# Kernel tuning notes

Hardware: AMD Instinct MI355X
Metric: run time of the kernel (lower is better)

The kernel has to match this reference:

```python
import jax, jax.numpy as jnp
import numpy as np

N_KNN = 16
BN_EPS = 1e-5


def conv1d(x, w, b):
    # x: [B, Cin, N], w: [Cout, Cin], b: [Cout] (1x1 Conv1d)
    return jnp.einsum('oc,bcn->bon', w, x) + b[None, :, None]


def conv2d(x, w, b):
    # x: [B, Cin, N, K], w: [Cout, Cin], b: [Cout] (1x1 Conv2d)
    return jnp.einsum('oc,bcnk->bonk', w, x) + b[None, :, None, None]


def bn2d(x, gamma, beta, mean, var):
    # eval-mode BatchNorm2d over channel axis 1
    scale = (gamma / jnp.sqrt(var + BN_EPS))[None, :, None, None]
    return (x - mean[None, :, None, None]) * scale + beta[None, :, None, None]


def knn_idx(pos, k):
    # pos: [B, 3, N] -> idx: [B, N, K] of k nearest neighbors (incl. self)
    p = jnp.swapaxes(pos, 1, 2)  # [B, N, 3]
    sq = jnp.sum(p * p, axis=-1)  # [B, N]
    d2 = sq[:, :, None] - 2.0 * jnp.einsum('bnd,bmd->bnm', p, p) + sq[:, None, :]
    _, idx = jax.lax.top_k(-d2, k)
    return idx


def group(x, idx):
    # x: [B, C, N], idx: [B, N, K] -> [B, C, N, K] (grouping_operation)
    return jax.vmap(lambda xb, ib: xb[:, ib])(x, idx)


def setup_inputs() -> dict:
    key = jax.random.key(0)
    B, C_OBJ, C_Q, N, DIM, PH, AM = 4, 512, 512, 4096, 128, 64, 4
    ks = jax.random.split(key, 32)
    r = lambda i, sh, s=0.05: jax.random.normal(ks[i], sh, jnp.float32) * s
    inp = {
        'obj_feature': jax.random.normal(ks[0], (B, C_OBJ, N), jnp.float32),
        'pos': jax.random.normal(ks[1], (B, 3, N), jnp.float32),
        'query_points': jax.random.normal(ks[2], (B, C_Q, N), jnp.float32),
        # linear_start_query / linear_start_obj
        'w_sq': r(3, (DIM, C_Q)), 'b_sq': r(4, (DIM,)),
        'w_so': r(5, (DIM, C_OBJ)), 'b_so': r(6, (DIM,)),
        # key / query / value 1x1 convs
        'w_k': r(7, (DIM, DIM)), 'b_k': r(8, (DIM,)),
        'w_q': r(9, (DIM, DIM)), 'b_q': r(10, (DIM,)),
        'w_v': r(11, (DIM, DIM)), 'b_v': r(12, (DIM,)),
        # pos_mlp: Conv2d(3->PH), BN, ReLU, Conv2d(PH->DIM)
        'w_p1': r(13, (PH, 3)), 'b_p1': r(14, (PH,)),
        'g_bn1': 1.0 + r(15, (PH,)), 'be_bn1': r(16, (PH,)),
        'm_bn1': r(17, (PH,)), 'v_bn1': 1.0 + 0.1 * jax.random.uniform(ks[18], (PH,), jnp.float32),
        'w_p2': r(19, (DIM, PH)), 'b_p2': r(20, (DIM,)),
        # attn_mlp: Conv2d(DIM->DIM*AM), BN, ReLU, Conv2d(DIM*AM->DIM)
        'w_a1': r(21, (DIM * AM, DIM)), 'b_a1': r(22, (DIM * AM,)),
        'g_bn2': 1.0 + r(23, (DIM * AM,)), 'be_bn2': r(24, (DIM * AM,)),
        'm_bn2': r(25, (DIM * AM,)), 'v_bn2': 1.0 + 0.1 * jax.random.uniform(ks[26], (DIM * AM,), jnp.float32),
        # linear_end
        'w_e': r(27, (C_OBJ, DIM)), 'b_e': r(28, (C_OBJ,)),
    }
    return inp


def reference(obj_feature, pos, query_points, w_sq, b_sq, w_so, b_so, w_k, b_k,
              w_q, b_q, w_v, b_v, w_p1, b_p1, g_bn1, be_bn1, m_bn1, v_bn1,
              w_p2, b_p2, w_a1, b_a1, g_bn2, be_bn2, m_bn2, v_bn2, w_e, b_e):
    qf = conv1d(query_points, w_sq, b_sq)          # [B, dim, N]
    f = conv1d(obj_feature, w_so, b_so)            # [B, dim, N]
    idx = knn_idx(jax.lax.stop_gradient(pos), N_KNN)  # [B, N, K]
    key_g = group(conv1d(f, w_k, b_k), idx)        # [B, dim, N, K]
    value = conv1d(f, w_v, b_v)                    # [B, dim, N]
    query = conv1d(qf, w_q, b_q)                   # [B, dim, N]
    qk_rel = query[:, :, :, None] - key_g          # [B, dim, N, K]
    pos_rel = pos[:, :, :, None] - group(pos, idx)  # [B, 3, N, K]
    pe = conv2d(jax.nn.relu(bn2d(conv2d(pos_rel, w_p1, b_p1), g_bn1, be_bn1, m_bn1, v_bn1)), w_p2, b_p2)
    attn = conv2d(jax.nn.relu(bn2d(conv2d(qk_rel + pe, w_a1, b_a1), g_bn2, be_bn2, m_bn2, v_bn2)), w_a2_placeholder := w_p2 * 0 + 0, b_p2 * 0) if False else None
    hidden = jax.nn.relu(bn2d(conv2d(qk_rel + pe, w_a1, b_a1), g_bn2, be_bn2, m_bn2, v_bn2))
    attn = jax.nn.softmax(conv2d(hidden, w_a2, b_a2), axis=-1)  # softmax over K
    v = value[:, :, :, None] + pe                  # [B, dim, N, K]
    agg = jnp.sum(attn * v, axis=-1)               # 'b c i j, b c i j -> b c i'
    return conv1d(agg, w_e, b_e)                   # [B, C_obj, N]

# fix: w_a2/b_a2 are parameters; re-declare reference cleanly to include them

def _setup_extra(inp):
    kk = jax.random.split(jax.random.key(7), 2)
    inp['w_a2'] = jax.random.normal(kk[0], (128, 512), jnp.float32) * 0.05
    inp['b_a2'] = jax.random.normal(kk[1], (128,), jnp.float32) * 0.05
    return inp

_orig_setup = setup_inputs

def setup_inputs():
    return _setup_extra(_orig_setup())


def reference(obj_feature, pos, query_points, w_sq, b_sq, w_so, b_so, w_k, b_k,
              w_q, b_q, w_v, b_v, w_p1, b_p1, g_bn1, be_bn1, m_bn1, v_bn1,
              w_p2, b_p2, w_a1, b_a1, g_bn2, be_bn2, m_bn2, v_bn2, w_a2, b_a2,
              w_e, b_e):
    qf = conv1d(query_points, w_sq, b_sq)
    f = conv1d(obj_feature, w_so, b_so)
    idx = knn_idx(jax.lax.stop_gradient(pos), N_KNN)
    key_g = group(conv1d(f, w_k, b_k), idx)
    value = conv1d(f, w_v, b_v)
    query = conv1d(qf, w_q, b_q)
    qk_rel = query[:, :, :, None] - key_g
    pos_rel = pos[:, :, :, None] - group(pos, idx)
    pe = conv2d(jax.nn.relu(bn2d(conv2d(pos_rel, w_p1, b_p1), g_bn1, be_bn1, m_bn1, v_bn1)), w_p2, b_p2)
    hidden = jax.nn.relu(bn2d(conv2d(qk_rel + pe, w_a1, b_a1), g_bn2, be_bn2, m_bn2, v_bn2))
    attn = jax.nn.softmax(conv2d(hidden, w_a2, b_a2), axis=-1)
    v = value[:, :, :, None] + pe
    agg = jnp.sum(attn * v, axis=-1)
    return conv1d(agg, w_e, b_e)
```

## Files before the change

kernel.cpp:

```cpp
#include <hip/hip_runtime.h>

typedef __bf16 bf16;
typedef __bf16 bf16x8 __attribute__((ext_vector_type(8)));
typedef __bf16 bf16x4 __attribute__((ext_vector_type(4)));
typedef __bf16 bf16x2 __attribute__((ext_vector_type(2)));
typedef float f32x4 __attribute__((ext_vector_type(4)));

#define MFMA16(a,b,c) __builtin_amdgcn_mfma_f32_16x16x32_bf16((a),(b),(c),0,0,0)

#define NPTS 4096
#define CIN 512
#define DIM 128
#define PH 64
#define HID 512

#define OFF_WQS 0u
#define OFF_WKO (128u*1024u)
#define OFF_WVO (256u*1024u)
#define OFF_BQS (384u*1024u)
#define OFF_BKO (385u*1024u)
#define OFF_BVO (386u*1024u)
#define OFF_S1  (387u*1024u)
#define OFF_T1  (388u*1024u)
#define OFF_S2  (389u*1024u)
#define OFF_T2  (391u*1024u)
#define OFF_CW  (400u*1024u)
#define OFF_QT  (1u<<20)
#define OFF_KT  (OFF_QT + (4u<<20))
#define OFF_VT  (OFF_QT + (8u<<20))
#define OFF_IDX (OFF_QT + (12u<<20))
#define WS_NEED (OFF_QT + (13u<<20))

struct P {
  const float* in[31];
  char* ws;
  float* out;
};

__global__ __launch_bounds__(256) void k_fold(P p) {
  int tid = blockIdx.x*256 + threadIdx.x;
  char* ws = p.ws;
  if (tid < 196608) {
    int m_id = tid >> 16, o = (tid >> 9) & 127, c = tid & 511;
    const float* A  = m_id==0 ? p.in[9] : (m_id==1 ? p.in[7] : p.in[11]);
    const float* Bm = (m_id==0) ? p.in[3] : p.in[5];
    float acc = 0.f;
    #pragma unroll 8
    for (int m=0;m<128;m++) acc += A[o*128+m] * Bm[m*512+c];
    bf16* outw = (bf16*)(ws + (m_id==0?OFF_WQS: m_id==1?OFF_WKO:OFF_WVO));
    outw[o*512+c] = (bf16)acc;
  } else if (tid < 196992) {
    int t = tid - 196608; int m_id = t >> 7, o = t & 127;
    const float* A  = m_id==0 ? p.in[9] : (m_id==1 ? p.in[7] : p.in[11]);
    const float* bb = (m_id==0) ? p.in[4] : p.in[6];
    const float* bs = m_id==0 ? p.in[10] : (m_id==1 ? p.in[8] : p.in[12]);
    float acc = bs[o];
    for (int m=0;m<128;m++) acc += A[o*128+m] * bb[m];
    float* ob = (float*)(ws + (m_id==0?OFF_BQS: m_id==1?OFF_BKO:OFF_BVO));
    ob[o] = acc;
  } else if (tid < 197056) {
    int i = tid - 196992;
    float s = p.in[15][i] * rsqrtf(p.in[18][i] + 1e-5f);
    ((float*)(ws+OFF_S1))[i] = s;
    ((float*)(ws+OFF_T1))[i] = (p.in[14][i] - p.in[17][i])*s + p.in[16][i];
  } else if (tid < 197568) {
    int i = tid - 197056;
    float s = p.in[23][i] * rsqrtf(p.in[26][i] + 1e-5f);
    ((float*)(ws+OFF_S2))[i] = s;
    ((float*)(ws+OFF_T2))[i] = (p.in[22][i] - p.in[25][i])*s + p.in[24][i];
  } else if (tid < 223168) {
    int e0 = (tid - 197568) * 8;
    const float* src; int base;
    if (e0 < 8192)        { src = p.in[19]; base = 0; }
    else if (e0 < 73728)  { src = p.in[21]; base = 8192; }
    else if (e0 < 139264) { src = p.in[29]; base = 73728; }
    else                  { src = p.in[27]; base = 139264; }
    const float* sp = src + (e0 - base);
    f32x4 a = *(const f32x4*)sp, b2 = *(const f32x4*)(sp+4);
    bf16x8 o8;
    o8[0]=(bf16)a[0]; o8[1]=(bf16)a[1]; o8[2]=(bf16)a[2]; o8[3]=(bf16)a[3];
    o8[4]=(bf16)b2[0]; o8[5]=(bf16)b2[1]; o8[6]=(bf16)b2[2]; o8[7]=(bf16)b2[3];
    *(bf16x8*)((bf16*)(ws+OFF_CW) + e0) = o8;
  }
}

__global__ __launch_bounds__(256) void k_knn(P p) {
  int lane = threadIdx.x & 63, w = threadIdx.x >> 6;
  int ig = blockIdx.x*4 + w;
  int b = ig >> 12, n = ig & 4095;
  const float* pb = p.in[1] + b*3*NPTS;
  float qx = pb[n], qy = pb[NPTS+n], qz = pb[2*NPTS+n];
  float sqn = __fadd_rn(__fadd_rn(__fmul_rn(qx,qx), __fmul_rn(qy,qy)), __fmul_rn(qz,qz));
  float d2a[64];
  #pragma unroll
  for (int t=0;t<64;t++) {
    int j = t*64 + lane;
    float xj=pb[j], yj=pb[NPTS+j], zj=pb[2*NPTS+j];
    float sqj = __fadd_rn(__fadd_rn(__fmul_rn(xj,xj), __fmul_rn(yj,yj)), __fmul_rn(zj,zj));
    float dot = __fadd_rn(__fadd_rn(__fmul_rn(qx,xj), __fmul_rn(qy,yj)), __fmul_rn(qz,zj));
    d2a[t] = __fadd_rn(__fsub_rn(sqn, __fmul_rn(2.f,dot)), sqj);
  }
  int* op = (int*)(p.ws + OFF_IDX) + ig*16;
  long long prev = -1ll;
  for (int r=0;r<16;r++) {
    long long best = 0x7fffffffffffffffll;
    #pragma unroll
    for (int t=0;t<64;t++) {
      long long key = ((long long)(int)__float_as_uint(d2a[t]) << 32) | (long long)(t*64+lane);
      if (key > prev && key < best) best = key;
    }
    #pragma unroll
    for (int off=32; off>0; off>>=1) {
      long long o = __shfl_xor(best, off);
      best = best < o ? best : o;
    }
    prev = best;
    if (lane==0) op[r] = (int)best & 4095;
  }
}

__global__ __launch_bounds__(256) void k_qkv(P p) {
  int mat = blockIdx.z, b = blockIdx.y, n0 = blockIdx.x*64;
  int tid = threadIdx.x, lane = tid&63, w = tid>>6;
  const float* in = (mat==0 ? p.in[2] : p.in[0]) + b*CIN*NPTS;
  const bf16* W = (const bf16*)(p.ws + (mat==0?OFF_WQS: mat==1?OFF_WKO:OFF_WVO));
  const float* bias = (const float*)(p.ws + (mat==0?OFF_BQS: mat==1?OFF_BKO:OFF_BVO));
  bf16* outT = (bf16*)(p.ws + (mat==0?OFF_QT: mat==1?OFF_KT:OFF_VT)) + (b*NPTS + n0)*DIM;
  __shared__ __align__(16) bf16 Bl[64*40];
  f32x4 acc[8] = {};
  for (int ks=0; ks<16; ks++) {
    int c0 = ks*32;
    {
      int cc = tid>>3, nn0 = (tid&7)*8;
      const float* sp = in + (c0+cc)*NPTS + n0 + nn0;
      f32x4 a = *(const f32x4*)sp, b2 = *(const f32x4*)(sp+4);
      Bl[(nn0+0)*40+cc]=(bf16)a[0];  Bl[(nn0+1)*40+cc]=(bf16)a[1];
      Bl[(nn0+2)*40+cc]=(bf16)a[2];  Bl[(nn0+3)*40+cc]=(bf16)a[3];
      Bl[(nn0+4)*40+cc]=(bf16)b2[0]; Bl[(nn0+5)*40+cc]=(bf16)b2[1];
      Bl[(nn0+6)*40+cc]=(bf16)b2[2]; Bl[(nn0+7)*40+cc]=(bf16)b2[3];
    }
    __syncthreads();
    int ncol = w*16 + (lane&15);
    bf16x8 bfr = *(const bf16x8*)(&Bl[ncol*40 + (lane>>4)*8]);
    #pragma unroll
    for (int ot=0;ot<8;ot++) {
      bf16x8 af = *(const bf16x8*)(W + (ot*16 + (lane&15))*CIN + c0 + (lane>>4)*8);
      acc[ot] = MFMA16(af, bfr, acc[ot]);
    }
    __syncthreads();
  }
  int o0 = (lane>>4)*4;
  int nloc = w*16 + (lane&15);
  #pragma unroll
  for (int ot=0;ot<8;ot++) {
    f32x4 bs = *(const f32x4*)(bias + ot*16 + o0);
    bf16x4 st;
    st[0]=(bf16)(acc[ot][0]+bs[0]); st[1]=(bf16)(acc[ot][1]+bs[1]);
    st[2]=(bf16)(acc[ot][2]+bs[2]); st[3]=(bf16)(acc[ot][3]+bs[3]);
    *(bf16x4*)(outT + nloc*DIM + ot*16 + o0) = st;
  }
}

__global__ __launch_bounds__(512) void k_fused(P p) {
  int b = blockIdx.y, pt0 = blockIdx.x*8;
  int tid=threadIdx.x, lane=tid&63, w=tid>>6;
  char* ws = p.ws;
  const bf16* qT = (const bf16*)(ws+OFF_QT) + b*NPTS*DIM;
  const bf16* kT = (const bf16*)(ws+OFF_KT) + b*NPTS*DIM;
  const bf16* vT = (const bf16*)(ws+OFF_VT) + b*NPTS*DIM;
  const int* idxg = (const int*)(ws+OFF_IDX) + (b*NPTS + pt0)*16;
  const bf16* wp2b = (const bf16*)(ws+OFF_CW);
  const bf16* wa1b = wp2b + 8192;
  const bf16* wa2b = wa1b + 65536;
  const bf16* web  = wa2b + 65536;
  __shared__ __align__(16) bf16 Xl[128*136];
  __shared__ __align__(16) bf16 HT[128*72];
  __shared__ __align__(16) bf16 aggl[16*136];
  __shared__ float prl[128][4];
  __shared__ int idxl[128];

  if (tid < 128) {
    int pt = tid>>4;
    int j = idxg[tid] & 4095;
    idxl[tid] = j;
    const float* pb = p.in[1] + b*3*NPTS;
    int n = pt0+pt;
    prl[tid][0] = pb[n]        - pb[j];
    prl[tid][1] = pb[NPTS+n]   - pb[NPTS+j];
    prl[tid][2] = pb[2*NPTS+n] - pb[2*NPTS+j];
  } else if (tid >= 256 && tid < 392) {
    f32x4 z = {};
    *(f32x4*)((char*)aggl + 2176 + (tid-256)*16) = z;
  }
  __syncthreads();

  {
    int col = tid & 127, mb = (tid>>7)*16;
    float r0=prl[col][0], r1=prl[col][1], r2=prl[col][2];
    const float* wp1 = p.in[13];
    const float* s1 = (const float*)(ws+OFF_S1);
    const float* t1 = (const float*)(ws+OFF_T1);
    #pragma unroll
    for (int i=0;i<16;i+=2) {
      int m = mb+i;
      float x0 = wp1[m*3]*r0   + wp1[m*3+1]*r1 + wp1[m*3+2]*r2;
      float x1 = wp1[m*3+3]*r0 + wp1[m*3+4]*r1 + wp1[m*3+5]*r2;
      bf16x2 pk;
      pk[0] = (bf16)fmaxf(0.f, x0*s1[m]   + t1[m]);
      pk[1] = (bf16)fmaxf(0.f, x1*s1[m+1] + t1[m+1]);
      *(bf16x2*)(&HT[col*72 + m]) = pk;
    }
  }
  __syncthreads();

  {
    f32x4 acc[8] = {};
    int crow = w*16 + (lane&15);
    #pragma unroll
    for (int ksx=0; ksx<2; ksx++) {
      int m0 = ksx*32 + (lane>>4)*8;
      bf16x8 af = *(const bf16x8*)(wp2b + crow*PH + m0);
      #pragma unroll
      for (int nt=0; nt<8; nt++) {
        int col = nt*16 + (lane&15);
        bf16x8 bfr = *(const bf16x8*)(&HT[col*72 + m0]);
        acc[nt] = MFMA16(af, bfr, acc[nt]);
      }
    }
    int c0 = w*16 + (lane>>4)*4;
    f32x4 bp4 = *(const f32x4*)(p.in[20] + c0);
    #pragma unroll
    for (int nt=0; nt<8; nt++) {
      int col = nt*16 + (lane&15);
      int j = idxl[col];
      int n = pt0 + nt;
      bf16x4 q4 = *(const bf16x4*)(qT + n*DIM + c0);
      bf16x4 k4 = *(const bf16x4*)(kT + j*DIM + c0);
      bf16x4 st;
      #pragma unroll
      for (int r=0;r<4;r++)
        st[r] = (bf16)((float)q4[r] - (float)k4[r] + acc[nt][r] + bp4[r]);
      *(bf16x4*)(&Xl[col*136 + c0]) = st;
    }
  }
  __syncthreads();

  f32x4 S[8] = {};
  const float* s2 = (const float*)(ws+OFF_S2);
  const float* t2 = (const float*)(ws+OFF_T2);
  for (int ch=0; ch<8; ch++) {
    f32x4 acc1[4] = {};
    int mtw = w & 3, nbase = (w>>2)*4;
    int hrow = ch*64 + mtw*16 + (lane&15);
    #pragma unroll
    for (int ksx=0; ksx<4; ksx++) {
      bf16x8 af = *(const bf16x8*)(wa1b + hrow*DIM + ksx*32 + (lane>>4)*8);
      #pragma unroll
      for (int i=0; i<4; i++) {
        int col = (nbase+i)*16 + (lane&15);
        bf16x8 bfr = *(const bf16x8*)(&Xl[col*136 + ksx*32 + (lane>>4)*8]);
        acc1[i] = MFMA16(af, bfr, acc1[i]);
      }
    }
    int h0 = ch*64 + mtw*16 + (lane>>4)*4;
    int h0loc = mtw*16 + (lane>>4)*4;
    f32x4 sv = *(const f32x4*)(s2 + h0);
    f32x4 tv = *(const f32x4*)(t2 + h0);
    #pragma unroll
    for (int i=0;i<4;i++) {
      int col = (nbase+i)*16 + (lane&15);
      bf16x4 st;
      st[0]=(bf16)fmaxf(0.f, acc1[i][0]*sv[0]+tv[0]);
      st[1]=(bf16)fmaxf(0.f, acc1[i][1]*sv[1]+tv[1]);
      st[2]=(bf16)fmaxf(0.f, acc1[i][2]*sv[2]+tv[2]);
      st[3]=(bf16)fmaxf(0.f, acc1[i][3]*sv[3]+tv[3]);
      *(bf16x4*)(&HT[col*72 + h0loc]) = st;
    }
    __syncthreads();
    int orow = w*16 + (lane&15);
    #pragma unroll
    for (int ksx=0; ksx<2; ksx++) {
      bf16x8 af = *(const bf16x8*)(wa2b + orow*HID + ch*64 + ksx*32 + (lane>>4)*8);
      #pragma unroll
      for (int nt=0; nt<8; nt++) {
        int col = nt*16 + (lane&15);
        bf16x8 bfr = *(const bf16x8*)(&HT[col*72 + ksx*32 + (lane>>4)*8]);
        S[nt] = MFMA16(af, bfr, S[nt]);
      }
    }
    __syncthreads();
  }

  {
    int c0 = w*16 + (lane>>4)*4;
    #pragma unroll
    for (int nt=0; nt<8; nt++) {
      f32x4 s = S[nt];
      float at[4];
      #pragma unroll
      for (int r=0;r<4;r++) {
        float mx = s[r];
        #pragma unroll
        for (int mk=8; mk; mk>>=1) mx = fmaxf(mx, __shfl_xor(mx, mk));
        float e = __expf(s[r]-mx);
        float sum = e;
        #pragma unroll
        for (int mk=8; mk; mk>>=1) sum += __shfl_xor(sum, mk);
        at[r] = e / sum;
      }
      int col = nt*16 + (lane&15);
      int j = idxl[col];
      int n = pt0 + nt;
      bf16x4 x4 = *(const bf16x4*)(&Xl[col*136 + c0]);
      bf16x4 q4 = *(const bf16x4*)(qT + n*DIM + c0);
      bf16x4 k4 = *(const bf16x4*)(kT + j*DIM + c0);
      bf16x4 v4 = *(const bf16x4*)(vT + n*DIM + c0);
      float ag[4];
      #pragma unroll
      for (int r=0;r<4;r++) {
        float vpe = (float)v4[r] + (float)x4[r] - (float)q4[r] + (float)k4[r];
        float cab = at[r]*vpe;
        #pragma unroll
        for (int mk=8; mk; mk>>=1) cab += __shfl_xor(cab, mk);
        ag[r] = cab;
      }
      if ((lane&15)==0) {
        bf16x4 st;
        st[0]=(bf16)ag[0]; st[1]=(bf16)ag[1]; st[2]=(bf16)ag[2]; st[3]=(bf16)ag[3];
        *(bf16x4*)(&aggl[nt*136 + c0]) = st;
      }
    }
  }
  __syncthreads();

  {
    const float* be = p.in[28];
    f32x4 acc5[4] = {};
    #pragma unroll
    for (int ksx=0; ksx<4; ksx++) {
      int pcol = lane&15;
      bf16x8 bfr = *(const bf16x8*)(&aggl[pcol*136 + ksx*32 + (lane>>4)*8]);
      #pragma unroll
      for (int i=0;i<4;i++) {
        int e = (w*4+i)*16 + (lane&15);
        bf16x8 af = *(const bf16x8*)(web + e*DIM + ksx*32 + (lane>>4)*8);
        acc5[i] = MFMA16(af, bfr, acc5[i]);
      }
    }
    int ptc = lane&15;
    if (ptc < 8) {
      int n = pt0 + ptc;
      #pragma unroll
      for (int i=0;i<4;i++) {
        int e0 = (w*4+i)*16 + (lane>>4)*4;
        f32x4 be4 = *(const f32x4*)(be + e0);
        #pragma unroll
        for (int r=0;r<4;r++)
          p.out[(b*CIN + e0+r)*NPTS + n] = acc5[i][r] + be4[r];
      }
    }
  }
}

extern "C" void kernel_launch(void* const* d_in, const int* in_sizes, int n_in,
                              void* d_out, int out_size, void* d_ws, size_t ws_size,
                              hipStream_t stream) {
  if (ws_size < WS_NEED || n_in < 31) return;
  P p;
  for (int i=0;i<31;i++) p.in[i] = (const float*)d_in[i];
  p.ws = (char*)d_ws;
  p.out = (float*)d_out;
  k_fold<<<872, 256, 0, stream>>>(p);
  k_knn<<<4096, 256, 0, stream>>>(p);
  k_qkv<<<dim3(64, 4, 3), 256, 0, stream>>>(p);
  k_fused<<<dim3(512, 4), 512, 0, stream>>>(p);
}
```

Measured before the change: 457.3 us.

## Rework kNN selection and retile attention MLP with 2D warp tiles and DPP reductions

The kNN kernel now stores distances as order-preserving 32-bit unsigned keys. Each round takes a single unsigned min scan and then clears the chosen element, replacing the previous 64-bit key comparisons against the last selected value. In the fused kernel, the attention MLP is retiled so each warp computes a 32x64 block over 128-wide hidden chunks (4 chunks instead of 8). This halves the barrier count and reuses each loaded B fragment across two A rows. Softmax and aggregation reductions use DPP row rotations instead of shuffles, at the cost of a larger HT shared buffer and a switch-based dynamic register clear.

After: 483.3 us. +5.7%, slower.

```diff
diff --git a/kernel.cpp b/kernel.cpp
--- a/kernel.cpp
+++ b/kernel.cpp
@@ -36,6 +36,16 @@
   char* ws;
   float* out;
 };
+
+template<int C> __device__ __forceinline__ float rorf(float x){
+  return __int_as_float(__builtin_amdgcn_mov_dpp(__float_as_int(x), 0x120|C, 0xF, 0xF, true));
+}
+__device__ __forceinline__ float red16max(float x){
+  x=fmaxf(x,rorf<1>(x)); x=fmaxf(x,rorf<2>(x)); x=fmaxf(x,rorf<4>(x)); x=fmaxf(x,rorf<8>(x)); return x;
+}
+__device__ __forceinline__ float red16sum(float x){
+  x+=rorf<1>(x); x+=rorf<2>(x); x+=rorf<4>(x); x+=rorf<8>(x); return x;
+}
 
 __global__ __launch_bounds__(256) void k_fold(P p) {
   int tid = blockIdx.x*256 + threadIdx.x;
@@ -91,31 +101,53 @@
   const float* pb = p.in[1] + b*3*NPTS;
   float qx = pb[n], qy = pb[NPTS+n], qz = pb[2*NPTS+n];
   float sqn = __fadd_rn(__fadd_rn(__fmul_rn(qx,qx), __fmul_rn(qy,qy)), __fmul_rn(qz,qz));
-  float d2a[64];
+  unsigned u[64];
   #pragma unroll
   for (int t=0;t<64;t++) {
     int j = t*64 + lane;
     float xj=pb[j], yj=pb[NPTS+j], zj=pb[2*NPTS+j];
     float sqj = __fadd_rn(__fadd_rn(__fmul_rn(xj,xj), __fmul_rn(yj,yj)), __fmul_rn(zj,zj));
     float dot = __fadd_rn(__fadd_rn(__fmul_rn(qx,xj), __fmul_rn(qy,yj)), __fmul_rn(qz,zj));
-    d2a[t] = __fadd_rn(__fsub_rn(sqn, __fmul_rn(2.f,dot)), sqj);
+    float d2 = __fadd_rn(__fsub_rn(sqn, __fmul_rn(2.f,dot)), sqj);
+    unsigned bbits = __float_as_uint(d2);
+    u[t] = bbits ^ (((unsigned)((int)bbits >> 31)) | 0x80000000u);
   }
   int* op = (int*)(p.ws + OFF_IDX) + ig*16;
-  long long prev = -1ll;
+  int tsel_s = 64; bool mine = false;
+  #pragma unroll 1
   for (int r=0;r<16;r++) {
-    long long best = 0x7fffffffffffffffll;
+    switch (tsel_s) {
+#define CLR(T) case T: u[T] = mine ? 0xFFFFFFFFu : u[T]; break;
+      CLR(0) CLR(1) CLR(2) CLR(3) CLR(4) CLR(5) CLR(6) CLR(7)
+      CLR(8) CLR(9) CLR(10) CLR(11) CLR(12) CLR(13) CLR(14) CLR(15)
+      CLR(16) CLR(17) CLR(18) CLR(19) CLR(20) CLR(21) CLR(22) CLR(23)
+      CLR(24) CLR(25) CLR(26) CLR(27) CLR(28) CLR(29) CLR(30) CLR(31)
+      CLR(32) CLR(33) CLR(34) CLR(35) CLR(36) CLR(37) CLR(38) CLR(39)
+      CLR(40) CLR(41) CLR(42) CLR(43) CLR(44) CLR(45) CLR(46) CLR(47)
+      CLR(48) CLR(49) CLR(50) CLR(51) CLR(52) CLR(53) CLR(54) CLR(55)
+      CLR(56) CLR(57) CLR(58) CLR(59) CLR(60) CLR(61) CLR(62) CLR(63)
+#undef CLR
+      default: break;
+    }
+    unsigned vmin = 0xFFFFFFFFu; int tmin = 0;
     #pragma unroll
     for (int t=0;t<64;t++) {
-      long long key = ((long long)(int)__float_as_uint(d2a[t]) << 32) | (long long)(t*64+lane);
-      if (key > prev && key < best) best = key;
-    }
+      bool lt = u[t] < vmin;
+      vmin = lt ? u[t] : vmin;
+      tmin = lt ? t : tmin;
+    }
+    int jmin = (tmin<<6) | lane;
     #pragma unroll
     for (int off=32; off>0; off>>=1) {
-      long long o = __shfl_xor(best, off);
-      best = best < o ? best : o;
-    }
-    prev = best;
-    if (lane==0) op[r] = (int)best & 4095;
+      unsigned vo = (unsigned)__shfl_xor((int)vmin, off);
+      int jo = __shfl_xor(jmin, off);
+      bool take = (vo < vmin) || (vo == vmin && (unsigned)jo < (unsigned)jmin);
+      vmin = take ? vo : vmin;
+      jmin = take ? jo : jmin;
+    }
+    if (lane==0) op[r] = jmin;
+    tsel_s = __builtin_amdgcn_readfirstlane(jmin >> 6);
+    mine = (lane == (jmin & 63));
   }
 }
 
@@ -162,29 +194,31 @@
 }
 
 __global__ __launch_bounds__(512) void k_fused(P p) {
-  int b = blockIdx.y, pt0 = blockIdx.x*8;
+  int bb = blockIdx.y, pt0 = blockIdx.x*8;
   int tid=threadIdx.x, lane=tid&63, w=tid>>6;
+  int c = lane&15, g = lane>>4;
   char* ws = p.ws;
-  const bf16* qT = (const bf16*)(ws+OFF_QT) + b*NPTS*DIM;
-  const bf16* kT = (const bf16*)(ws+OFF_KT) + b*NPTS*DIM;
-  const bf16* vT = (const bf16*)(ws+OFF_VT) + b*NPTS*DIM;
-  const int* idxg = (const int*)(ws+OFF_IDX) + (b*NPTS + pt0)*16;
+  const bf16* qT = (const bf16*)(ws+OFF_QT) + bb*NPTS*DIM;
+  const bf16* kT = (const bf16*)(ws+OFF_KT) + bb*NPTS*DIM;
+  const bf16* vT = (const bf16*)(ws+OFF_VT) + bb*NPTS*DIM;
+  const int* idxg = (const int*)(ws+OFF_IDX) + (bb*NPTS + pt0)*16;
   const bf16* wp2b = (const bf16*)(ws+OFF_CW);
   const bf16* wa1b = wp2b + 8192;
   const bf16* wa2b = wa1b + 65536;
   const bf16* web  = wa2b + 65536;
+  const float* s2 = (const float*)(ws+OFF_S2);
+  const float* t2 = (const float*)(ws+OFF_T2);
   __shared__ __align__(16) bf16 Xl[128*136];
-  __shared__ __align__(16) bf16 HT[128*72];
+  __shared__ __align__(16) bf16 HT[128*136];
   __shared__ __align__(16) bf16 aggl[16*136];
   __shared__ float prl[128][4];
   __shared__ int idxl[128];
 
   if (tid < 128) {
-    int pt = tid>>4;
     int j = idxg[tid] & 4095;
     idxl[tid] = j;
-    const float* pb = p.in[1] + b*3*NPTS;
-    int n = pt0+pt;
+    const float* pb = p.in[1] + bb*3*NPTS;
+    int n = pt0 + (tid>>4);
     prl[tid][0] = pb[n]        - pb[j];
     prl[tid][1] = pb[NPTS+n]   - pb[NPTS+j];
     prl[tid][2] = pb[2*NPTS+n] - pb[2*NPTS+j];
@@ -208,30 +242,30 @@
       bf16x2 pk;
       pk[0] = (bf16)fmaxf(0.f, x0*s1[m]   + t1[m]);
       pk[1] = (bf16)fmaxf(0.f, x1*s1[m+1] + t1[m+1]);
-      *(bf16x2*)(&HT[col*72 + m]) = pk;
+      *(bf16x2*)(&HT[col*136 + m]) = pk;
     }
   }
   __syncthreads();
 
   {
     f32x4 acc[8] = {};
-    int crow = w*16 + (lane&15);
+    int crow = w*16 + c;
     #pragma unroll
     for (int ksx=0; ksx<2; ksx++) {
-      int m0 = ksx*32 + (lane>>4)*8;
+      int m0 = ksx*32 + g*8;
       bf16x8 af = *(const bf16x8*)(wp2b + crow*PH + m0);
       #pragma unroll
       for (int nt=0; nt<8; nt++) {
-        int col = nt*16 + (lane&15);
-        bf16x8 bfr = *(const bf16x8*)(&HT[col*72 + m0]);
+        int col = nt*16 + c;
+        bf16x8 bfr = *(const bf16x8*)(&HT[col*136 + m0]);
         acc[nt] = MFMA16(af, bfr, acc[nt]);
       }
     }
-    int c0 = w*16 + (lane>>4)*4;
+    int c0 = w*16 + g*4;
     f32x4 bp4 = *(const f32x4*)(p.in[20] + c0);
     #pragma unroll
     for (int nt=0; nt<8; nt++) {
-      int col = nt*16 + (lane&15);
+      int col = nt*16 + c;
       int j = idxl[col];
       int n = pt0 + nt;
       bf16x4 q4 = *(const bf16x4*)(qT + n*DIM + c0);
@@ -245,89 +279,83 @@
   }
   __syncthreads();
 
-  f32x4 S[8] = {};
-  const float* s2 = (const float*)(ws+OFF_S2);
-  const float* t2 = (const float*)(ws+OFF_T2);
-  for (int ch=0; ch<8; ch++) {
-    f32x4 acc1[4] = {};
-    int mtw = w & 3, nbase = (w>>2)*4;
-    int hrow = ch*64 + mtw*16 + (lane&15);
-    #pragma unroll
-    for (int ksx=0; ksx<4; ksx++) {
-      bf16x8 af = *(const bf16x8*)(wa1b + hrow*DIM + ksx*32 + (lane>>4)*8);
-      #pragma unroll
-      for (int i=0; i<4; i++) {
-        int col = (nbase+i)*16 + (lane&15);
-        bf16x8 bfr = *(const bf16x8*)(&Xl[col*136 + ksx*32 + (lane>>4)*8]);
-        acc1[i] = MFMA16(af, bfr, acc1[i]);
-      }
-    }
-    int h0 = ch*64 + mtw*16 + (lane>>4)*4;
-    int h0loc = mtw*16 + (lane>>4)*4;
-    f32x4 sv = *(const f32x4*)(s2 + h0);
-    f32x4 tv = *(const f32x4*)(t2 + h0);
-    #pragma unroll
-    for (int i=0;i<4;i++) {
-      int col = (nbase+i)*16 + (lane&15);
-      bf16x4 st;
-      st[0]=(bf16)fmaxf(0.f, acc1[i][0]*sv[0]+tv[0]);
-      st[1]=(bf16)fmaxf(0.f, acc1[i][1]*sv[1]+tv[1]);
-      st[2]=(bf16)fmaxf(0.f, acc1[i][2]*sv[2]+tv[2]);
-      st[3]=(bf16)fmaxf(0.f, acc1[i][3]*sv[3]+tv[3]);
-      *(bf16x4*)(&HT[col*72 + h0loc]) = st;
+  f32x4 S[2][4] = {{{},{},{},{}},{{},{},{},{}}};
+  int h32 = (w&3)*32, ch64 = (w>>2)*64;
+  #pragma unroll 1
+  for (int cc4=0; cc4<4; cc4++) {
+    int hbase = cc4*128;
+    f32x4 acc[2][4] = {{{},{},{},{}},{{},{},{},{}}};
+    #pragma unroll
+    for (int ksx=0;ksx<4;ksx++) {
+      int k0 = ksx*32 + g*8;
+      bf16x8 af0 = *(const bf16x8*)(wa1b + (hbase+h32+c)*DIM + k0);
+      bf16x8 af1 = *(const bf16x8*)(wa1b + (hbase+h32+16+c)*DIM + k0);
+      #pragma unroll
+      for (int cg=0;cg<4;cg++) {
+        bf16x8 bfr = *(const bf16x8*)(&Xl[(ch64+cg*16+c)*136 + k0]);
+        acc[0][cg] = MFMA16(af0, bfr, acc[0][cg]);
+        acc[1][cg] = MFMA16(af1, bfr, acc[1][cg]);
+      }
+    }
+    #pragma unroll
+    for (int mt2=0;mt2<2;mt2++) {
+      int hg = hbase + h32 + mt2*16 + g*4;
+      f32x4 sv = *(const f32x4*)(s2+hg), tv = *(const f32x4*)(t2+hg);
+      int hloc = h32 + mt2*16 + g*4;
+      #pragma unroll
+      for (int cg=0;cg<4;cg++) {
+        int col = ch64+cg*16+c;
+        bf16x4 st;
+        st[0]=(bf16)fmaxf(0.f, acc[mt2][cg][0]*sv[0]+tv[0]);
+        st[1]=(bf16)fmaxf(0.f, acc[mt2][cg][1]*sv[1]+tv[1]);
+        st[2]=(bf16)fmaxf(0.f, acc[mt2][cg][2]*sv[2]+tv[2]);
+        st[3]=(bf16)fmaxf(0.f, acc[mt2][cg][3]*sv[3]+tv[3]);
+        *(bf16x4*)(&HT[col*136 + hloc]) = st;
+      }
     }
     __syncthreads();
-    int orow = w*16 + (lane&15);
-    #pragma unroll
-    for (int ksx=0; ksx<2; ksx++) {
-      bf16x8 af = *(const bf16x8*)(wa2b + orow*HID + ch*64 + ksx*32 + (lane>>4)*8);
-      #pragma unroll
-      for (int nt=0; nt<8; nt++) {
-        int col = nt*16 + (lane&15);
-        bf16x8 bfr = *(const bf16x8*)(&HT[col*72 + ksx*32 + (lane>>4)*8]);
-        S[nt] = MFMA16(af, bfr, S[nt]);
+    #pragma unroll
+    for (int ksx=0;ksx<4;ksx++) {
+      int k0 = ksx*32 + g*8;
+      bf16x8 af0 = *(const bf16x8*)(wa2b + (h32+c)*HID + hbase + k0);
+      bf16x8 af1 = *(const bf16x8*)(wa2b + (h32+16+c)*HID + hbase + k0);
+      #pragma unroll
+      for (int cg=0;cg<4;cg++) {
+        bf16x8 bfr = *(const bf16x8*)(&HT[(ch64+cg*16+c)*136 + k0]);
+        S[0][cg] = MFMA16(af0, bfr, S[0][cg]);
+        S[1][cg] = MFMA16(af1, bfr, S[1][cg]);
       }
     }
     __syncthreads();
   }
 
-  {
-    int c0 = w*16 + (lane>>4)*4;
-    #pragma unroll
-    for (int nt=0; nt<8; nt++) {
-      f32x4 s = S[nt];
-      float at[4];
+  #pragma unroll
+  for (int mt2=0;mt2<2;mt2++) {
+    #pragma unroll
+    for (int cg=0;cg<4;cg++) {
+      int ptl = (w>>2)*4 + cg;
+      int pt = pt0 + ptl;
+      int col = ch64 + cg*16 + c;
+      int j = idxl[col];
+      int chb = h32 + mt2*16 + g*4;
+      bf16x4 x4 = *(const bf16x4*)(&Xl[col*136 + chb]);
+      bf16x4 q4 = *(const bf16x4*)(qT + pt*DIM + chb);
+      bf16x4 k4 = *(const bf16x4*)(kT + j*DIM + chb);
+      bf16x4 v4 = *(const bf16x4*)(vT + pt*DIM + chb);
+      float agv[4];
       #pragma unroll
       for (int r=0;r<4;r++) {
-        float mx = s[r];
-        #pragma unroll
-        for (int mk=8; mk; mk>>=1) mx = fmaxf(mx, __shfl_xor(mx, mk));
-        float e = __expf(s[r]-mx);
-        float sum = e;
-        #pragma unroll
-        for (int mk=8; mk; mk>>=1) sum += __shfl_xor(sum, mk);
-        at[r] = e / sum;
-      }
-      int col = nt*16 + (lane&15);
-      int j = idxl[col];
-      int n = pt0 + nt;
-      bf16x4 x4 = *(const bf16x4*)(&Xl[col*136 + c0]);
-      bf16x4 q4 = *(const bf16x4*)(qT + n*DIM + c0);
-      bf16x4 k4 = *(const bf16x4*)(kT + j*DIM + c0);
-      bf16x4 v4 = *(const bf16x4*)(vT + n*DIM + c0);
-      float ag[4];
-      #pragma unroll
-      for (int r=0;r<4;r++) {
+        float s = S[mt2][cg][r];
+        float mx = red16max(s);
+        float e = __expf(s-mx);
+        float sm = red16sum(e);
+        float at = e/sm;
         float vpe = (float)v4[r] + (float)x4[r] - (float)q4[r] + (float)k4[r];
-        float cab = at[r]*vpe;
-        #pragma unroll
-        for (int mk=8; mk; mk>>=1) cab += __shfl_xor(cab, mk);
-        ag[r] = cab;
-      }
-      if ((lane&15)==0) {
-        bf16x4 st;
-        st[0]=(bf16)ag[0]; st[1]=(bf16)ag[1]; st[2]=(bf16)ag[2]; st[3]=(bf16)ag[3];
-        *(bf16x4*)(&aggl[nt*136 + c0]) = st;
+        agv[r] = red16sum(at*vpe);
+      }
+      if (c==0) {
+        bf16x4 st; st[0]=(bf16)agv[0]; st[1]=(bf16)agv[1]; st[2]=(bf16)agv[2]; st[3]=(bf16)agv[3];
+        *(bf16x4*)(&aggl[ptl*136 + chb]) = st;
       }
     }
   }
@@ -338,25 +366,24 @@
     f32x4 acc5[4] = {};
     #pragma unroll
     for (int ksx=0; ksx<4; ksx++) {
-      int pcol = lane&15;
-      bf16x8 bfr = *(const bf16x8*)(&aggl[pcol*136 + ksx*32 + (lane>>4)*8]);
+      int pcol = c;
+      bf16x8 bfr = *(const bf16x8*)(&aggl[pcol*136 + ksx*32 + g*8]);
       #pragma unroll
       for (int i=0;i<4;i++) {
-        int e = (w*4+i)*16 + (lane&15);
-        bf16x8 af = *(const bf16x8*)(web + e*DIM + ksx*32 + (lane>>4)*8);
+        int e = (w*4+i)*16 + c;
+        bf16x8 af = *(const bf16x8*)(web + e*DIM + ksx*32 + g*8);
         acc5[i] = MFMA16(af, bfr, acc5[i]);
       }
     }
-    int ptc = lane&15;
-    if (ptc < 8) {
-      int n = pt0 + ptc;
+    if (c < 8) {
+      int n = pt0 + c;
       #pragma unroll
       for (int i=0;i<4;i++) {
-        int e0 = (w*4+i)*16 + (lane>>4)*4;
+        int e0 = (w*4+i)*16 + g*4;
         f32x4 be4 = *(const f32x4*)(be + e0);
         #pragma unroll
         for (int r=0;r<4;r++)
-          p.out[(b*CIN + e0+r)*NPTS + n] = acc5[i][r] + be4[r];
+          p.out[(bb*CIN + e0+r)*NPTS + n] = acc5[i][r] + be4[r];
       }
     }
   }
```
